# Performance work log

Hardware: AMD Instinct MI355X
Metric: run time of the kernel (lower is better)

Reference implementation:

```python
import math
import jax, jax.numpy as jnp
import numpy as np
from jax import lax

DIM = 4096
N_STEPS = 12 * 4096  # ceil(log2(4096)) * 4096
SEED = 2024


def make_walk_params(seed, n_steps, dim):
    """Deterministic (i, j, cos, sin) schedule for one Kac random walk."""
    key = jax.random.key(seed)
    ki, kj, kt = jax.random.split(key, 3)
    i = jax.random.randint(ki, (n_steps,), 0, dim)
    j = jax.random.randint(kj, (n_steps,), 0, dim - 1)
    j = j + (j >= i).astype(j.dtype)  # ensure j != i
    theta = jax.random.uniform(kt, (n_steps,), minval=0.0, maxval=2.0 * np.pi)
    return (i.astype(jnp.int32), j.astype(jnp.int32),
            jnp.cos(theta).astype(jnp.float32), jnp.sin(theta).astype(jnp.float32))


def kac_walk(x, i_idx, j_idx, cos_t, sin_t):
    """Apply n_steps sequential 2x2 Givens rotations to columns of x [N, dim]."""
    def step(x, p):
        ii, jj, c, s = p
        xi = x[:, ii]
        xj = x[:, jj]
        x = x.at[:, ii].set(c * xi + s * xj)
        x = x.at[:, jj].set(c * xj - s * xi)
        return x, None
    x, _ = lax.scan(step, x, (i_idx, j_idx, cos_t, sin_t))
    return x


def setup_inputs() -> dict:
    key = jax.random.key(0)
    kx, kw, kb, kv = jax.random.split(key, 4)
    x = jax.random.normal(kx, (1, 512, DIM), dtype=jnp.float32)
    W = jax.random.normal(kw, (DIM, DIM), dtype=jnp.float32) / math.sqrt(DIM)
    b = jax.random.normal(kb, (DIM,), dtype=jnp.float32) * 0.01
    vec = jax.random.normal(kv, (DIM,), dtype=jnp.float32) / math.sqrt(DIM)
    i1, j1, c1, s1 = make_walk_params(SEED * 2, N_STEPS, DIM)
    i2, j2, c2, s2 = make_walk_params(SEED * 2 + 1, N_STEPS, DIM)
    return {"x": x, "W": W, "b": b, "vec": vec,
            "i1": i1, "j1": j1, "c1": c1, "s1": s1,
            "i2": i2, "j2": j2, "c2": c2, "s2": s2}


def reference(x, W, b, vec, i1, j1, c1, s1, i2, j2, c2, s2):
    # frozen base layer: y = x @ W.T + b
    y = jnp.einsum('bsd,od->bso', x, W) + b
    # Kac adapter path
    x2d = x.reshape(-1, DIM)                 # [N, dim]
    yp = kac_walk(x2d, i1, j1, c1, s1)
    yp = vec * yp                            # per-coordinate scale
    yp = kac_walk(yp, i2, j2, c2, s2)
    return y + yp.reshape(y.shape)
```

## Files before the change

kernel.cpp:

```cpp
#include <hip/hip_runtime.h>


#define DIM    4096
#define ROWS   512
#define NSTEPS 49152
#define WSTEPS 8192
#define NW2    (NSTEPS / WSTEPS)
#define NSLOT  (2 * NW2)
#define NSG    16
#define CHUNK  128
#define WVN    4
#define PWC    96
#define SLOTREC (WVN * PWC * CHUNK)
#define MAXR   96
#define PADI   4096
#define PADJ   4097
#define KT     1024
#define SPT    (WSTEPS / KT)
#define NCVW   1024
#define NCVX   128
#define SMEMB  33664

typedef short  short8 __attribute__((ext_vector_type(8)));
typedef __bf16 bf16x8 __attribute__((ext_vector_type(8)));
typedef float  f32x4  __attribute__((ext_vector_type(4)));

__device__ inline short f2bf(float f) {
    unsigned u = __builtin_bit_cast(unsigned, f);
    u += 0x7FFFu + ((u >> 16) & 1u);
    return (short)(u >> 16);
}
__device__ inline short8 pack8(float4 a, float4 b) {
    short8 r;
    r[0] = f2bf(a.x); r[1] = f2bf(a.y); r[2] = f2bf(a.z); r[3] = f2bf(a.w);
    r[4] = f2bf(b.x); r[5] = f2bf(b.y); r[6] = f2bf(b.z); r[7] = f2bf(b.w);
    return r;
}
__device__ inline float bitf(unsigned u) { return __builtin_bit_cast(float, u); }
__device__ inline float2 ldrw(const float2* rw, int boff) {
    return *(const float2*)((const char*)rw + boff);
}
__device__ inline void strw(float2* rw, int boff, float2 v) {
    *(float2*)((char*)rw + boff) = v;
}
__device__ inline void gl16(const short* g, short* l) {
    __builtin_amdgcn_global_load_lds((const __attribute__((address_space(1))) unsigned*)g,
                                     (__attribute__((address_space(3))) unsigned*)l, 16, 0, 0);
}

__global__ __launch_bounds__(KT) void kfused(
    const int* __restrict__ i1, const int* __restrict__ j1,
    const float* __restrict__ c1, const float* __restrict__ s1,
    const int* __restrict__ i2, const int* __restrict__ j2,
    const float* __restrict__ c2, const float* __restrict__ s2,
    uint4* __restrict__ recs, int* __restrict__ nlvls, unsigned* __restrict__ lvmeta_g,
    int doconv, const float* __restrict__ W, const float* __restrict__ X,
    short* __restrict__ wb, short* __restrict__ xb) {

    if (blockIdx.x >= NSLOT) {
        if (!doconv) return;
        const int cb = blockIdx.x - NSLOT;
        const float* src; short* dst; size_t base;
        if (cb < NCVW) { src = W; dst = wb; base = (size_t)cb * 16384; }
        else           { src = X; dst = xb; base = (size_t)(cb - NCVW) * 16384; }
        const size_t o = base + (size_t)threadIdx.x * 16;
        const float4* s4 = (const float4*)(src + o);
        const float4 a0 = s4[0], a1 = s4[1], a2 = s4[2], a3 = s4[3];
        *(short8*)(dst + o)     = pack8(a0, a1);
        *(short8*)(dst + o + 8) = pack8(a2, a3);
        return;
    }

    __shared__ unsigned tbl[DIM];
    __shared__ unsigned spair[WSTEPS];
    __shared__ unsigned lvrk[WSTEPS];
    __shared__ int lcnt[MAXR * NSG];
    __shared__ unsigned lvpk[MAXR], wvbase[MAXR];
    __shared__ unsigned char serf[MAXR];
    __shared__ int nlvlsh;

    const int b    = blockIdx.x;
    const int walk = b / NW2;
    const int w    = b % NW2;
    const int t    = threadIdx.x;
    const int gb   = w * WSTEPS;
    const int sg   = t >> 6;

    const int*   I = walk ? i2 : i1;
    const int*   J = walk ? j2 : j1;
    const float* C = walk ? c2 : c1;
    const float* S = walk ? s2 : s1;

    uint4* slotp = recs + (size_t)b * SLOTREC;
    {
        const uint4 padrec = { (unsigned)(PADI * 8), 0x3F800000u, 0u, (unsigned)(PADJ * 8) };
        for (int k = t; k < SLOTREC; k += KT) slotp[k] = padrec;
    }
    for (int s = t; s < WSTEPS; s += KT)
        spair[s] = (unsigned)I[gb + s] | ((unsigned)J[gb + s] << 16);
    for (int k = t; k < DIM; k += KT) tbl[k] = 0xFFFFFFFFu;
    for (int k = t; k < MAXR * NSG; k += KT) lcnt[k] = 0;
    if (t < MAXR) serf[t] = 0;
    if (t == 0) nlvlsh = 1;
    __syncthreads();

    unsigned pmask = (1u << SPT) - 1u;
    for (int rr = 0; rr < MAXR; ++rr) {
        const unsigned rk = (unsigned)(MAXR - 1 - rr) << 13;
#pragma unroll
        for (int q = 0; q < SPT; ++q)
            if (pmask & (1u << q)) {
                const int s = q * KT + t;
                const unsigned sp = spair[s];
                const unsigned key = rk | (unsigned)s;
                atomicMin(&tbl[sp & 0xFFFFu], key);
                atomicMin(&tbl[sp >> 16], key);
            }
        __syncthreads();
#pragma unroll
        for (int q = 0; q < SPT; ++q)
            if (pmask & (1u << q)) {
                const int s = q * KT + t;
                const unsigned sp = spair[s];
                const unsigned key = rk | (unsigned)s;
                if (tbl[sp & 0xFFFFu] == key && tbl[sp >> 16] == key) {
                    const int rank = atomicAdd(&lcnt[rr * NSG + sg], 1);
                    lvrk[s] = ((unsigned)rank << 8) | (unsigned)rr;
                    pmask &= ~(1u << q);
                }
            }
        const int np = __syncthreads_count(pmask != 0);
        if (np == 0) break;
    }
#pragma unroll
    for (int q = 0; q < SPT; ++q)
        if (pmask & (1u << q)) {
            const int s = q * KT + t;
            const int rank = atomicAdd(&lcnt[(MAXR - 1) * NSG + sg], 1);
            lvrk[s] = ((unsigned)rank << 8) | (unsigned)(MAXR - 1);
        }
    __syncthreads();

    if (t < MAXR) {
        int run = 0;
        for (int g = 0; g < NSG; ++g) {
            const int v = lcnt[t * NSG + g];
            lcnt[t * NSG + g] = run;
            run += v;
        }
        const int nch = (run + 127) >> 7;
        unsigned pk = 0;
        if (run > 0 && nch <= 2) { serf[t] = 1; pk = (unsigned)nch; }
        else {
#pragma unroll
            for (int wv = 0; wv < WVN; ++wv)
                pk |= (unsigned)((nch + (WVN - 1 - wv)) >> 2) << (8 * wv);
        }
        lvpk[t] = pk;
        if (run > 0) atomicMax(&nlvlsh, t + 1);
    }
    __syncthreads();
    if (t < 64) {
        const int l = t;
        const unsigned w1 = lvpk[l];
        unsigned x1 = w1;
        for (int off = 1; off < 64; off <<= 1) {
            const unsigned v = (unsigned)__shfl_up((int)x1, off);
            if (l >= off) x1 += v;
        }
        wvbase[l] = x1 - w1;
        const unsigned seg1 = (unsigned)__shfl((int)x1, 63);
        const int l2 = 64 + (l & 31);
        const unsigned w2 = lvpk[l2];
        unsigned x2 = w2;
        for (int off = 1; off < 32; off <<= 1) {
            const unsigned v = (unsigned)__shfl_up((int)x2, off);
            if ((l & 31) >= off) x2 += v;
        }
        if (l < 32) wvbase[l2] = seg1 + x2 - w2;
    }
    __syncthreads();
    if (t < MAXR - 1) {
        if (serf[t] && serf[t + 1]) lvpk[t] |= 0x80000000u;
    }
    __syncthreads();
    if (t == 0) nlvls[b] = nlvlsh;
    if (t < MAXR) lvmeta_g[b * MAXR + t] = lvpk[t];

#pragma unroll
    for (int q = 0; q < SPT; ++q) {
        const int s = q * KT + t;
        const unsigned v = lvrk[s];
        const int lvl  = (int)(v & 0xFFu);
        const int rank = (int)(v >> 8) + lcnt[lvl * NSG + sg];
        const int cl   = rank >> 7;
        const int pos  = rank & 127;
        int wv2, wc2;
        if (serf[lvl]) { wv2 = 0; wc2 = cl; }
        else           { wv2 = cl & (WVN - 1); wc2 = cl >> 2; }
        const int pch = (int)((wvbase[lvl] >> (8 * wv2)) & 0xFFu) + wc2;
        if (pch < PWC) {
            const unsigned sp = spair[s];
            const int g = gb + s;
            uint4 r;
            r.x = (sp & 0xFFFFu) * 8u;
            r.y = __builtin_bit_cast(unsigned, C[g]);
            r.z = __builtin_bit_cast(unsigned, S[g]);
            r.w = (sp >> 16) * 8u;
            slotp[((size_t)wv2 * PWC + pch) * CHUNK + pos] = r;
        }
    }
}

__device__ void walk_body(char* smem, int pr,
                          const float* __restrict__ X, const float* __restrict__ vec,
                          const uint4* __restrict__ recs, const int* __restrict__ nlvls,
                          const unsigned* __restrict__ lvmeta_g,
                          float* __restrict__ dstbuf, int directadd) {
    float2* rw = (float2*)smem;
    unsigned* lvm = (unsigned*)(smem + (DIM + 2) * 8);
    const int tid  = threadIdx.x;
    const int wv   = tid >> 6;
    const int lane = tid & 63;
    const int rA   = pr * 2, rB = pr * 2 + 1;

    {
        const float4* xa = (const float4*)(X + (size_t)rA * DIM);
        const float4* xb = (const float4*)(X + (size_t)rB * DIM);
        for (int c4 = tid; c4 < DIM / 4; c4 += 256) {
            const float4 a = xa[c4], b = xb[c4];
            rw[c4 * 4 + 0] = make_float2(a.x, b.x);
            rw[c4 * 4 + 1] = make_float2(a.y, b.y);
            rw[c4 * 4 + 2] = make_float2(a.z, b.z);
            rw[c4 * 4 + 3] = make_float2(a.w, b.w);
        }
        if (tid < 2) rw[DIM + tid] = make_float2(0.f, 0.f);
    }

    for (int slot = 0; slot < NSLOT; ++slot) {
        if (slot == NW2) {
            __syncthreads();
            const float4* v4 = (const float4*)vec;
            for (int c4 = tid; c4 < DIM / 4; c4 += 256) {
                const float4 v = v4[c4];
#pragma unroll
                for (int q = 0; q < 4; ++q) {
                    float2 tv = rw[c4 * 4 + q];
                    const float sc = (q == 0) ? v.x : (q == 1) ? v.y : (q == 2) ? v.z : v.w;
                    tv.x *= sc; tv.y *= sc;
                    rw[c4 * 4 + q] = tv;
                }
            }
        }
        if (tid < MAXR) lvm[tid] = lvmeta_g[slot * MAXR + tid];
        const int nlvl = nlvls[slot];
        __syncthreads();

        const uint4* wbase = recs + (size_t)slot * SLOTREC + (size_t)wv * (PWC * CHUNK);
        uint4 r0A = wbase[lane],       r0B = wbase[64 + lane];
        uint4 r1A = wbase[128 + lane], r1B = wbase[192 + lane];
        uint4 r2A = wbase[256 + lane], r2B = wbase[320 + lane];
        int t = 0;

        for (int lvl = 0; lvl < nlvl; ++lvl) {
            const unsigned mm = lvm[lvl];
            int n = (int)((mm >> (wv * 8)) & 0xFFu);
            if (wv == 3) n &= 0x7F;
            for (int it = 0; it < n; ++it) {
                int kc = t + 3; if (kc > PWC - 1) kc = PWC - 1;
                const uint4 mA = wbase[(size_t)kc * CHUNK + lane];
                const uint4 mB = wbase[(size_t)kc * CHUNK + 64 + lane];

                const int   ia = (int)r0A.x, ja = (int)r0A.w;
                const int   ib = (int)r0B.x, jb = (int)r0B.w;
                const float ca = bitf(r0A.y), sa = bitf(r0A.z);
                const float cb = bitf(r0B.y), sb = bitf(r0B.z);
                const float2 gai = ldrw(rw, ia), gaj = ldrw(rw, ja);
                const float2 gbi = ldrw(rw, ib), gbj = ldrw(rw, jb);

                float2 wia, wja, wib, wjb;
                wia.x = fmaf(ca, gai.x,  sa * gaj.x);
                wia.y = fmaf(ca, gai.y,  sa * gaj.y);
                wja.x = fmaf(ca, gaj.x, -sa * gai.x);
                wja.y = fmaf(ca, gaj.y, -sa * gai.y);
                wib.x = fmaf(cb, gbi.x,  sb * gbj.x);
                wib.y = fmaf(cb, gbi.y,  sb * gbj.y);
                wjb.x = fmaf(cb, gbj.x, -sb * gbi.x);
                wjb.y = fmaf(cb, gbj.y, -sb * gbi.y);
                strw(rw, ia, wia); strw(rw, ja, wja);
                strw(rw, ib, wib); strw(rw, jb, wjb);

                r0A = r1A; r0B = r1B;
                r1A = r2A; r1B = r2B;
                r2A = mA;  r2B = mB;
                ++t;
            }
            if (!(mm & 0x80000000u)) {
                __builtin_amdgcn_sched_barrier(0);
                asm volatile("s_waitcnt lgkmcnt(0)" ::: "memory");
                __builtin_amdgcn_s_barrier();
                __builtin_amdgcn_sched_barrier(0);
            }
        }
    }

    float4* oa = (float4*)(dstbuf + (size_t)rA * DIM);
    float4* ob = (float4*)(dstbuf + (size_t)rB * DIM);
    for (int c4 = tid; c4 < DIM / 4; c4 += 256) {
        const float2 p0 = rw[c4 * 4 + 0], p1 = rw[c4 * 4 + 1];
        const float2 p2 = rw[c4 * 4 + 2], p3 = rw[c4 * 4 + 3];
        float4 ta, tb;
        if (directadd) { ta = oa[c4]; tb = ob[c4]; }
        else           { ta = (float4){0,0,0,0}; tb = (float4){0,0,0,0}; }
        ta.x += p0.x; ta.y += p1.x; ta.z += p2.x; ta.w += p3.x;
        tb.x += p0.y; tb.y += p1.y; tb.z += p2.y; tb.w += p3.y;
        oa[c4] = ta; ob[c4] = tb;
    }
}

__device__ void gemm_body(char* smem, int bid,
                          const short* __restrict__ Xb, const short* __restrict__ Wb,
                          const float* __restrict__ bias, float* __restrict__ out,
                          float* __restrict__ parts, int nks) {
    short* As = (short*)smem;
    short* Bs = As + 128 * 64;
    const int ks   = bid % nks;
    const int tile = bid / nks;
    const int bm   = (tile >> 5) * 128;
    const int bn   = (tile & 31) * 128;
    const int tid  = threadIdx.x;
    const int lane = tid & 63;
    const int wv   = tid >> 6;
    const int wr   = (wv >> 1) * 64;
    const int wc   = (wv & 1) * 64;
    const int fr   = lane & 15;
    const int ke   = (lane >> 4) * 8;

    f32x4 acc[4][4];
#pragma unroll
    for (int m = 0; m < 4; ++m)
#pragma unroll
        for (int n = 0; n < 4; ++n) acc[m][n] = (f32x4){0.f, 0.f, 0.f, 0.f};

    const int lrow = lane >> 3;
    const int scol = (((lane & 7) ^ (lrow & 7)) << 3);
    const short* gx = Xb + (size_t)(bm + wv * 32 + lrow) * DIM + scol;
    const short* gw = Wb + (size_t)(bn + wv * 32 + lrow) * DIM + scol;
    short* lA = As + wv * 2048;
    short* lB = Bs + wv * 2048;

    const int nkt   = (DIM / 64) / nks;
    const int kbase = ks * (DIM / nks);
    for (int kt = 0; kt < nkt; ++kt) {
        const int k0 = kbase + kt * 64;
        __syncthreads();
#pragma unroll
        for (int q = 0; q < 4; ++q) {
            gl16(gx + (size_t)(q * 8) * DIM + k0, lA + q * 512);
            gl16(gw + (size_t)(q * 8) * DIM + k0, lB + q * 512);
        }
        __syncthreads();
#pragma unroll
        for (int kk = 0; kk < 64; kk += 32) {
            const int sb = (kk + ke) >> 3;
            short8 af[4], bf[4];
#pragma unroll
            for (int m = 0; m < 4; ++m) {
                const int R = wr + m * 16 + fr;
                af[m] = *(const short8*)&As[R * 64 + ((sb ^ (R & 7)) << 3)];
            }
#pragma unroll
            for (int n = 0; n < 4; ++n) {
                const int R = wc + n * 16 + fr;
                bf[n] = *(const short8*)&Bs[R * 64 + ((sb ^ (R & 7)) << 3)];
            }
#pragma unroll
            for (int m = 0; m < 4; ++m)
#pragma unroll
                for (int n = 0; n < 4; ++n)
                    acc[m][n] = __builtin_amdgcn_mfma_f32_16x16x32_bf16(
                        __builtin_bit_cast(bf16x8, af[m]),
                        __builtin_bit_cast(bf16x8, bf[n]),
                        acc[m][n], 0, 0, 0);
        }
    }
    float* dst = ks ? (parts + (size_t)(ks - 1) * ROWS * DIM) : out;
#pragma unroll
    for (int n = 0; n < 4; ++n) {
        const int col = bn + wc + n * 16 + fr;
        const float bv = ks ? 0.f : bias[col];
#pragma unroll
        for (int m = 0; m < 4; ++m) {
            const int rbase = bm + wr + m * 16 + (lane >> 4) * 4;
#pragma unroll
            for (int r = 0; r < 4; ++r)
                dst[(size_t)(rbase + r) * DIM + col] = acc[m][n][r] + bv;
        }
    }
}

__global__ __launch_bounds__(256) void kboth(
    const float* __restrict__ X, const float* __restrict__ vec,
    const uint4* __restrict__ recs, const int* __restrict__ nlvls,
    const unsigned* __restrict__ lvmeta_g, float* __restrict__ walkbuf,
    const short* __restrict__ Xb, const short* __restrict__ Wb,
    const float* __restrict__ bias, float* __restrict__ out,
    float* __restrict__ parts, int nks) {
    __shared__ __align__(16) char smem[SMEMB];
    if (blockIdx.x < ROWS / 2)
        walk_body(smem, blockIdx.x, X, vec, recs, nlvls, lvmeta_g, walkbuf, 0);
    else
        gemm_body(smem, blockIdx.x - ROWS / 2, Xb, Wb, bias, out, parts, nks);
}

__global__ __launch_bounds__(256) void kadd(float* __restrict__ out,
                                            const float* __restrict__ walkbuf,
                                            const float* __restrict__ parts, int nparts) {
    const size_t N = (size_t)ROWS * DIM / 4;
    const size_t i0 = (size_t)blockIdx.x * 256 + threadIdx.x;
    float4* o4 = (float4*)out;
    const float4* w4 = (const float4*)walkbuf;
    const float4* p4 = (const float4*)parts;
    for (size_t i = i0; i < N; i += (size_t)gridDim.x * 256) {
        float4 t = o4[i];
        const float4 s = w4[i];
        t.x += s.x; t.y += s.y; t.z += s.z; t.w += s.w;
        for (int p = 0; p < nparts; ++p) {
            const float4 a = p4[i + (size_t)p * N];
            t.x += a.x; t.y += a.y; t.z += a.z; t.w += a.w;
        }
        o4[i] = t;
    }
}

#define LDT 72
__global__ __launch_bounds__(256) void kgemm_small(const float* __restrict__ X, const float* __restrict__ W,
                                                   const float* __restrict__ bias, float* __restrict__ out) {
    __shared__ short As[64 * LDT];
    __shared__ short Bs[128 * LDT];
    const int tid  = threadIdx.x;
    const int bn   = (blockIdx.x & 31) * 128;
    const int bm   = (blockIdx.x >> 5) * 64;
    const int lane = tid & 63;
    const int wv   = tid >> 6;
    const int wr   = (wv >> 1) * 32;
    const int wc   = (wv & 1) * 64;
    const int fr   = lane & 15;
    const int ke   = (lane >> 4) * 8;

    f32x4 acc[2][4];
#pragma unroll
    for (int m = 0; m < 2; ++m)
#pragma unroll
        for (int n = 0; n < 4; ++n) acc[m][n] = (f32x4){0.f, 0.f, 0.f, 0.f};

    const int tr = tid >> 2;
    const int tc = (tid & 3) << 4;

    for (int kt = 0; kt < DIM / 64; ++kt) {
        const int k0 = kt * 64;
        float4 ra[4], rb[2][4];
        {
            const float4* ga = (const float4*)(X + (size_t)(bm + tr) * DIM + k0 + tc);
#pragma unroll
            for (int q = 0; q < 4; ++q) ra[q] = ga[q];
#pragma unroll
            for (int h = 0; h < 2; ++h) {
                const float4* gw = (const float4*)(W + (size_t)(bn + h * 64 + tr) * DIM + k0 + tc);
#pragma unroll
                for (int q = 0; q < 4; ++q) rb[h][q] = gw[q];
            }
        }
        __syncthreads();
        *(short8*)&As[tr * LDT + tc]     = pack8(ra[0], ra[1]);
        *(short8*)&As[tr * LDT + tc + 8] = pack8(ra[2], ra[3]);
#pragma unroll
        for (int h = 0; h < 2; ++h) {
            *(short8*)&Bs[(h * 64 + tr) * LDT + tc]     = pack8(rb[h][0], rb[h][1]);
            *(short8*)&Bs[(h * 64 + tr) * LDT + tc + 8] = pack8(rb[h][2], rb[h][3]);
        }
        __syncthreads();
#pragma unroll
        for (int kk = 0; kk < 64; kk += 32) {
            short8 af[2], bf[4];
#pragma unroll
            for (int m = 0; m < 2; ++m)
                af[m] = *(const short8*)&As[(wr + m * 16 + fr) * LDT + kk + ke];
#pragma unroll
            for (int n = 0; n < 4; ++n)
                bf[n] = *(const short8*)&Bs[(wc + n * 16 + fr) * LDT + kk + ke];
#pragma unroll
            for (int m = 0; m < 2; ++m)
#pragma unroll
                for (int n = 0; n < 4; ++n)
                    acc[m][n] = __builtin_amdgcn_mfma_f32_16x16x32_bf16(
                        __builtin_bit_cast(bf16x8, af[m]),
                        __builtin_bit_cast(bf16x8, bf[n]),
                        acc[m][n], 0, 0, 0);
        }
    }
#pragma unroll
    for (int n = 0; n < 4; ++n) {
        const int col = bn + wc + n * 16 + fr;
        const float bv = bias[col];
#pragma unroll
        for (int m = 0; m < 2; ++m) {
            const int rbase = bm + wr + m * 16 + (lane >> 4) * 4;
#pragma unroll
            for (int r = 0; r < 4; ++r)
                out[(size_t)(rbase + r) * DIM + col] = acc[m][n][r] + bv;
        }
    }
}

__global__ __launch_bounds__(256) void kwalk_fb(const float* __restrict__ X, const float* __restrict__ vec,
                                                const uint4* __restrict__ recs, const int* __restrict__ nlvls,
                                                const unsigned* __restrict__ lvmeta_g,
                                                float* __restrict__ out) {
    __shared__ __align__(16) char smem[SMEMB];
    walk_body(smem, blockIdx.x, X, vec, recs, nlvls, lvmeta_g, out, 1);
}

extern "C" void kernel_launch(void* const* d_in, const int* in_sizes, int n_in,
                              void* d_out, int out_size, void* d_ws, size_t ws_size,
                              hipStream_t stream) {
    const float* X    = (const float*)d_in[0];
    const float* W    = (const float*)d_in[1];
    const float* bias = (const float*)d_in[2];
    const float* vec  = (const float*)d_in[3];
    const int*   i1   = (const int*)d_in[4];
    const int*   j1   = (const int*)d_in[5];
    const float* c1   = (const float*)d_in[6];
    const float* s1   = (const float*)d_in[7];
    const int*   i2   = (const int*)d_in[8];
    const int*   j2   = (const int*)d_in[9];
    const float* c2   = (const float*)d_in[10];
    const float* s2   = (const float*)d_in[11];
    float* out = (float*)d_out;

    const size_t RD         = (size_t)ROWS * DIM * 4;
    const size_t WBB        = (size_t)DIM * DIM * 2;
    const size_t XBB        = (size_t)ROWS * DIM * 2;
    const size_t recs_bytes = (size_t)NSLOT * SLOTREC * 16;
    const size_t off_lvm    = recs_bytes + 1024;
    const size_t off_parts  = recs_bytes + 16384;

    int nks = 0;
    size_t off_wb = 0;
    {
        const size_t need4 = off_parts + 3 * RD + WBB + XBB + RD;
        const size_t need2 = off_parts + 1 * RD + WBB + XBB + RD;
        if      (ws_size >= need4) { nks = 4; off_wb = off_parts + 3 * RD; }
        else if (ws_size >= need2) { nks = 2; off_wb = off_parts + 1 * RD; }
    }

    uint4*    recs   = (uint4*)d_ws;
    int*      nlvlsb = (int*)((char*)d_ws + recs_bytes);
    unsigned* lvmeta = (unsigned*)((char*)d_ws + off_lvm);
    float*    parts  = (float*)((char*)d_ws + off_parts);
    short*    wbuf   = (short*)((char*)d_ws + off_wb);
    short*    xbuf   = (short*)((char*)d_ws + off_wb + WBB);
    float*    wkbuf  = (float*)((char*)d_ws + off_wb + WBB + XBB);
    const bool bf = (nks > 0);

    hipLaunchKernelGGL(kfused, dim3(NSLOT + (bf ? (NCVW + NCVX) : 0)), dim3(KT), 0, stream,
                       i1, j1, c1, s1, i2, j2, c2, s2, recs, nlvlsb, lvmeta,
                       bf ? 1 : 0, W, X, wbuf, xbuf);
    if (bf) {
        hipLaunchKernelGGL(kboth, dim3(ROWS / 2 + 128 * nks), dim3(256), 0, stream,
                           X, vec, recs, nlvlsb, lvmeta, wkbuf,
                           xbuf, wbuf, bias, out, parts, nks);
        hipLaunchKernelGGL(kadd, dim3(512), dim3(256), 0, stream,
                           out, wkbuf, parts, nks - 1);
    } else {
        hipLaunchKernelGGL(kgemm_small, dim3(256), dim3(256), 0, stream, X, W, bias, out);
        hipLaunchKernelGGL(kwalk_fb, dim3(ROWS / 2), dim3(256), 0, stream,
                           X, vec, recs, nlvlsb, lvmeta, out);
    }
}
```

Before: 213.3 us.

## Build slot records via shared inverse map, writing only used chunks contiguously

The schedule-building kernel no longer pre-fills the whole slot record buffer with padding and then scatters records. It builds an inverse position-to-step map in shared memory (reusing the tbl/spair pool), then writes each used chunk contiguously, with padding where a position has no step. This removes the full-buffer pad write and the scattered global stores, at the cost of extra syncs, gathered global reads of I/J/C/S, and an INVCAP bound that could silently drop records if capacity is exceeded.

```diff
diff --git a/kernel.cpp b/kernel.cpp
--- a/kernel.cpp
+++ b/kernel.cpp
@@ -20,6 +20,7 @@
 #define NCVW   1024
 #define NCVX   128
 #define SMEMB  33664
+#define INVCAP ((DIM + WSTEPS) * 2)
 
 typedef short  short8 __attribute__((ext_vector_type(8)));
 typedef __bf16 bf16x8 __attribute__((ext_vector_type(8)));
@@ -71,13 +72,17 @@
         return;
     }
 
-    __shared__ unsigned tbl[DIM];
-    __shared__ unsigned spair[WSTEPS];
+    __shared__ unsigned pool[DIM + WSTEPS];
     __shared__ unsigned lvrk[WSTEPS];
     __shared__ int lcnt[MAXR * NSG];
     __shared__ unsigned lvpk[MAXR], wvbase[MAXR];
     __shared__ unsigned char serf[MAXR];
     __shared__ int nlvlsh;
+    __shared__ unsigned totpk;
+    __shared__ int ucnt4[WVN], sbase4[WVN];
+
+    unsigned* tbl   = pool;
+    unsigned* spair = pool + DIM;
 
     const int b    = blockIdx.x;
     const int walk = b / NW2;
@@ -92,10 +97,7 @@
     const float* S = walk ? s2 : s1;
 
     uint4* slotp = recs + (size_t)b * SLOTREC;
-    {
-        const uint4 padrec = { (unsigned)(PADI * 8), 0x3F800000u, 0u, (unsigned)(PADJ * 8) };
-        for (int k = t; k < SLOTREC; k += KT) slotp[k] = padrec;
-    }
+
     for (int s = t; s < WSTEPS; s += KT)
         spair[s] = (unsigned)I[gb + s] | ((unsigned)J[gb + s] << 16);
     for (int k = t; k < DIM; k += KT) tbl[k] = 0xFFFFFFFFu;
@@ -178,15 +180,29 @@
             if ((l & 31) >= off) x2 += v;
         }
         if (l < 32) wvbase[l2] = seg1 + x2 - w2;
-    }
-    __syncthreads();
+        if (l == 31) totpk = seg1 + x2;
+    }
+    __syncthreads();
+    if (t < WVN) {
+        int u = (int)((totpk >> (8 * t)) & 0xFFu);
+        ucnt4[t] = (u > PWC) ? PWC : u;
+    }
     if (t < MAXR - 1) {
         if (serf[t] && serf[t + 1]) lvpk[t] |= 0x80000000u;
     }
     __syncthreads();
-    if (t == 0) nlvls[b] = nlvlsh;
+    if (t == 0) {
+        sbase4[0] = 0;
+        for (int v = 1; v < WVN; ++v) sbase4[v] = sbase4[v - 1] + ucnt4[v - 1];
+        nlvls[b] = nlvlsh;
+    }
     if (t < MAXR) lvmeta_g[b * MAXR + t] = lvpk[t];
-
+    __syncthreads();
+
+    const int usedtot = sbase4[WVN - 1] + ucnt4[WVN - 1];
+    for (int k = t; k < usedtot * 64; k += KT) pool[k] = 0xFFFFFFFFu;
+    __syncthreads();
+    unsigned short* inv = (unsigned short*)pool;
 #pragma unroll
     for (int q = 0; q < SPT; ++q) {
         const int s = q * KT + t;
@@ -199,15 +215,29 @@
         if (serf[lvl]) { wv2 = 0; wc2 = cl; }
         else           { wv2 = cl & (WVN - 1); wc2 = cl >> 2; }
         const int pch = (int)((wvbase[lvl] >> (8 * wv2)) & 0xFFu) + wc2;
-        if (pch < PWC) {
-            const unsigned sp = spair[s];
-            const int g = gb + s;
-            uint4 r;
-            r.x = (sp & 0xFFFFu) * 8u;
-            r.y = __builtin_bit_cast(unsigned, C[g]);
-            r.z = __builtin_bit_cast(unsigned, S[g]);
-            r.w = (sp >> 16) * 8u;
-            slotp[((size_t)wv2 * PWC + pch) * CHUNK + pos] = r;
+        if (pch < ucnt4[wv2]) {
+            const int ipos = (sbase4[wv2] + pch) * 128 + pos;
+            if (ipos < INVCAP) inv[ipos] = (unsigned short)s;
+        }
+    }
+    __syncthreads();
+
+    const uint4 padrec = { (unsigned)(PADI * 8), 0x3F800000u, 0u, (unsigned)(PADJ * 8) };
+    for (int wv = 0; wv < WVN; ++wv) {
+        const int npos = ucnt4[wv] * 128;
+        const int ibase = sbase4[wv] * 128;
+        uint4* dst = slotp + (size_t)wv * (PWC * CHUNK);
+        for (int p = t; p < npos; p += KT) {
+            const unsigned s = inv[ibase + p];
+            uint4 r = padrec;
+            if (s != 0xFFFFu) {
+                const int g = gb + (int)s;
+                r.x = (unsigned)(I[g] * 8);
+                r.y = __builtin_bit_cast(unsigned, C[g]);
+                r.z = __builtin_bit_cast(unsigned, S[g]);
+                r.w = (unsigned)(J[g] * 8);
+            }
+            dst[p] = r;
         }
     }
 }
```

Result: faster. 205.4 us (-3.7%).
